# Kernel tuning notes

Hardware: AMD Instinct MI355X
Metric: run time of the kernel (lower is better)

Reference implementation:

```python
import jax, jax.numpy as jnp
import numpy as np

B, A, L, M, E = 4096, 64, 16, 4, 10
K = (4, 16, 32)
Q = (2, 4, 6)
P = (32, 128, 256)


def setup_inputs() -> dict:
    key = jax.random.key(0)
    ks = iter(jax.random.split(key, 32))
    inp = {}
    inp['x'] = jax.random.normal(next(ks), (B, A, L, M), dtype=jnp.float32)
    inp['y'] = jax.random.uniform(next(ks), (B, E), dtype=jnp.float32)
    inp['w1'] = jax.random.normal(next(ks), (E, K[0], Q[0], A), dtype=jnp.float32) / (K[0] * Q[0])
    inp['w2'] = jax.random.normal(next(ks), (E, K[1], Q[1], A), dtype=jnp.float32) / (K[1] * Q[1])
    inp['w3'] = jax.random.normal(next(ks), (E, K[2], Q[2], A), dtype=jnp.float32) / (K[2] * Q[2])
    inp['coeff1'] = jax.random.normal(next(ks), (P[0],), dtype=jnp.float32)
    inp['coeff2'] = jax.random.normal(next(ks), (P[1],), dtype=jnp.float32)
    inp['coeff3'] = jax.random.normal(next(ks), (P[2],), dtype=jnp.float32)
    ri = lambda n, hi: jax.random.randint(next(ks), (n,), 0, hi, dtype=jnp.int32)
    inp['i1'] = ri(P[0], L); inp['l1'] = ri(P[0], M)
    inp['k1'] = ri(P[0], K[0]); inp['q1'] = ri(P[0], Q[0])
    inp['i2'] = ri(P[1], L); inp['j2'] = ri(P[1], L)
    inp['l2'] = ri(P[1], M); inp['m2'] = ri(P[1], M)
    inp['k2'] = ri(P[1], K[1]); inp['q2'] = ri(P[1], Q[1])
    inp['i3'] = ri(P[2], L); inp['j3'] = ri(P[2], L); inp['f3'] = ri(P[2], L)
    inp['l3'] = ri(P[2], M); inp['m3'] = ri(P[2], M); inp['g3'] = ri(P[2], M)
    inp['k3'] = ri(P[2], K[2]); inp['q3'] = ri(P[2], Q[2])
    return inp


def _forward(x, y, w1, w2, w3, coeff1, coeff2, coeff3,
             i1, l1, k1, q1,
             i2, j2, l2, m2, k2, q2,
             i3, j3, f3, l3, m3, g3, k3, q3):
    # element-mixed weights: [B, K, Q, A]
    wy1 = jnp.einsum('ekqa,be->bkqa', w1, y)
    wy2 = jnp.einsum('ekqa,be->bkqa', w2, y)
    wy3 = jnp.einsum('ekqa,be->bkqa', w3, y)
    # sparse path contraction (equivalent to dense 'ik,lq,ekqa,bail,be->ba' etc.)
    g1 = jnp.transpose(wy1[:, k1, q1, :], (0, 2, 1))          # [B, A, P1]
    t1 = jnp.einsum('bap,p->ba', x[:, :, i1, l1] * g1, coeff1)
    g2 = jnp.transpose(wy2[:, k2, q2, :], (0, 2, 1))          # [B, A, P2]
    t2 = jnp.einsum('bap,p->ba', x[:, :, i2, l2] * x[:, :, j2, m2] * g2, coeff2)
    g3_ = jnp.transpose(wy3[:, k3, q3, :], (0, 2, 1))         # [B, A, P3]
    t3 = jnp.einsum('bap,p->ba',
                    x[:, :, i3, l3] * x[:, :, j3, m3] * x[:, :, f3, g3] * g3_,
                    coeff3)
    return t1 + t2 + t3  # [B, A] (scalar irrep_out -> flattened view)


def reference(x, y, w1, w2, w3, coeff1, coeff2, coeff3,
              i1, l1, k1, q1,
              i2, j2, l2, m2, k2, q2,
              i3, j3, f3, l3, m3, g3, k3, q3):
    return _forward(x, y, w1, w2, w3, coeff1, coeff2, coeff3,
                    i1, l1, k1, q1,
                    i2, j2, l2, m2, k2, q2,
                    i3, j3, f3, l3, m3, g3, k3, q3)
```

## Files before the change

### kernel.cpp

```cpp
#include <hip/hip_runtime.h>
#include <hip/hip_bf16.h>

typedef _Float16 f16x8 __attribute__((ext_vector_type(8)));
typedef _Float16 f16x4 __attribute__((ext_vector_type(4)));
typedef float    f32x4 __attribute__((ext_vector_type(4)));

constexpr int BB  = 4096;
constexpr int AA  = 64;
constexpr int ED  = 10;
constexpr int P1N = 32, P2N = 128, P3N = 256;
constexpr int PT  = 416;
constexpr int NKS = 13;
constexpr int BCH = 64;
constexpr int NCH = 4;

__global__ void build_tables_kernel(
    const float* __restrict__ w1, const float* __restrict__ w2, const float* __restrict__ w3,
    const float* __restrict__ c1, const float* __restrict__ c2, const float* __restrict__ c3,
    const int* __restrict__ k1, const int* __restrict__ q1,
    const int* __restrict__ k2, const int* __restrict__ q2,
    const int* __restrict__ k3, const int* __restrict__ q3,
    const int* __restrict__ i1, const int* __restrict__ l1,
    const int* __restrict__ i2, const int* __restrict__ j2,
    const int* __restrict__ l2, const int* __restrict__ m2,
    const int* __restrict__ i3, const int* __restrict__ j3,
    const int* __restrict__ f3, const int* __restrict__ l3,
    const int* __restrict__ m3, const int* __restrict__ g3,
    _Float16* __restrict__ cwb, unsigned* __restrict__ idxs) {
  if (blockIdx.x == AA * NKS) {
    for (int p = threadIdx.x; p < PT; p += 64) {
      unsigned sa, sb = 64, sc = 64;
      if (p < P1N) {
        sa = i1[p] * 4 + l1[p];
      } else if (p < P1N + P2N) {
        int pp = p - P1N;
        sa = i2[pp] * 4 + l2[pp];
        sb = j2[pp] * 4 + m2[pp];
      } else {
        int pp = p - P1N - P2N;
        sa = i3[pp] * 4 + l3[pp];
        sb = j3[pp] * 4 + m3[pp];
        sc = f3[pp] * 4 + g3[pp];
      }
      idxs[p] = (sa * 8) | ((sb * 8) << 10) | ((sc * 8) << 20);
    }
    return;
  }
  const int a  = blockIdx.x & 63;
  const int ks = blockIdx.x >> 6;
  const int l  = threadIdx.x;
  const int grp = l >> 4, e = l & 15;
  const int aq = a >> 2, ch = a & 3;
  _Float16* dst = cwb + ((((size_t)aq * NKS + ks) * 64 + l) * 4 + ch) * 8;
  #pragma unroll
  for (int j = 0; j < 8; ++j) {
    const int p = ks * 32 + grp * 8 + j;
    float v = 0.f;
    if (e < ED) {
      const float* w; float coeff; int k, q, K, Q;
      if (p < P1N)            { w = w1; coeff = c1[p]; k = k1[p]; q = q1[p]; K = 4;  Q = 2; }
      else if (p < P1N + P2N) { int pp = p - P1N;       w = w2; coeff = c2[pp]; k = k2[pp]; q = q2[pp]; K = 16; Q = 4; }
      else                    { int pp = p - P1N - P2N; w = w3; coeff = c3[pp]; k = k3[pp]; q = q3[pp]; K = 32; Q = 6; }
      v = coeff * w[(((size_t)e * K + k) * Q + q) * AA + a];
    }
    dst[j] = (_Float16)v;
  }
}

template <int NF, int KS>
__device__ __forceinline__ void kstep(
    const char* __restrict__ rowb, const uint4* ip,
    const f16x8* __restrict__ cwq,
    f32x4& ac0, f32x4& ac1, f32x4& ac2, f32x4& ac3) {
  const uint4 iA = ip[KS * 8 + 0];
  const uint4 iB = ip[KS * 8 + 1];
  const f16x8* c = cwq + KS * 256;
  const f16x8 b0 = c[0];
  const f16x8 b1 = c[1];
  const f16x8 b2 = c[2];
  const f16x8 b3 = c[3];
  const unsigned pks[8] = {iA.x, iA.y, iA.z, iA.w, iB.x, iB.y, iB.z, iB.w};
  f16x8 af0, af1, af2, af3;
  #pragma unroll
  for (int jh = 0; jh < 2; ++jh) {
    f16x4 g0[4], g1[4], g2[4];
    #pragma unroll
    for (int j = 0; j < 4; ++j) {
      const unsigned pk = pks[jh * 4 + j];
      g0[j] = *(const f16x4*)(rowb + (pk & 1023u));
      if (NF >= 2) g1[j] = *(const f16x4*)(rowb + ((pk >> 10) & 1023u));
      if (NF >= 3) g2[j] = *(const f16x4*)(rowb + (pk >> 20));
    }
    #pragma unroll
    for (int j = 0; j < 4; ++j) {
      f16x4 v = g0[j];
      if (NF >= 2) v = v * g1[j];
      if (NF >= 3) v = v * g2[j];
      const int jj = jh * 4 + j;
      af0[jj] = v[0]; af1[jj] = v[1]; af2[jj] = v[2]; af3[jj] = v[3];
    }
  }
  ac0 = __builtin_amdgcn_mfma_f32_16x16x32_f16(af0, b0, ac0, 0, 0, 0);
  ac1 = __builtin_amdgcn_mfma_f32_16x16x32_f16(af1, b1, ac1, 0, 0, 0);
  ac2 = __builtin_amdgcn_mfma_f32_16x16x32_f16(af2, b2, ac2, 0, 0, 0);
  ac3 = __builtin_amdgcn_mfma_f32_16x16x32_f16(af3, b3, ac3, 0, 0, 0);
}

__global__ __launch_bounds__(256, 4)
void contract_kernel(const float* __restrict__ x, const float* __restrict__ y,
                     const unsigned* __restrict__ idxs,
                     const f16x8* __restrict__ cwb,
                     float* __restrict__ out) {
  __shared__ f16x4 xls[BCH][65];
  __shared__ float yls[BCH][17];
  __shared__ uint4 ils[PT / 4];

  const int t  = threadIdx.x;
  const int aq = blockIdx.x & 15;
  const int a0 = aq * NCH;
  const int b0 = (blockIdx.x >> 4) * BCH;
  const int wv = t >> 6, l = t & 63, grp = l >> 4, er = l & 15;
  const int r0 = wv * 16;

  {
    const uint4* gip = (const uint4*)idxs;
    for (int u = l; u < PT / 4; u += 64) ils[u] = gip[u];
  }

  #pragma unroll
  for (int i = 0; i < 4; ++i) {
    const int row = r0 + i * 4 + (l >> 4);
    const int s   = (l & 15) * 4;
    const float* xb = x + (size_t)(b0 + row) * 4096 + a0 * 64 + s;
    const float4 L0 = *(const float4*)(xb);
    const float4 L1 = *(const float4*)(xb + 64);
    const float4 L2 = *(const float4*)(xb + 128);
    const float4 L3 = *(const float4*)(xb + 192);
    f16x4 v0, v1, v2, v3;
    v0[0] = (_Float16)L0.x; v0[1] = (_Float16)L1.x; v0[2] = (_Float16)L2.x; v0[3] = (_Float16)L3.x;
    v1[0] = (_Float16)L0.y; v1[1] = (_Float16)L1.y; v1[2] = (_Float16)L2.y; v1[3] = (_Float16)L3.y;
    v2[0] = (_Float16)L0.z; v2[1] = (_Float16)L1.z; v2[2] = (_Float16)L2.z; v2[3] = (_Float16)L3.z;
    v3[0] = (_Float16)L0.w; v3[1] = (_Float16)L1.w; v3[2] = (_Float16)L2.w; v3[3] = (_Float16)L3.w;
    xls[row][s + 0] = v0;
    xls[row][s + 1] = v1;
    xls[row][s + 2] = v2;
    xls[row][s + 3] = v3;
  }
  if (l < 16) {
    f16x4 one;
    one[0] = one[1] = one[2] = one[3] = (_Float16)1.0f;
    xls[r0 + l][64] = one;
    const float* yb = y + (size_t)(b0 + r0 + l) * ED;
    #pragma unroll
    for (int e = 0; e < ED; ++e) yls[r0 + l][e] = yb[e];
    #pragma unroll
    for (int e = ED; e < 16; ++e) yls[r0 + l][e] = 0.f;
  }

  const char* __restrict__ rowb = (const char*)&xls[r0 + er][0];
  const f16x8* __restrict__ cwq = cwb + (size_t)aq * NKS * 256 + (size_t)l * 4;
  const uint4* ip = &ils[grp * 2];

  f32x4 a0A = {0.f, 0.f, 0.f, 0.f}, a1A = a0A, a2A = a0A, a3A = a0A;
  f32x4 a0B = a0A, a1B = a0A, a2B = a0A, a3B = a0A;

  #define SA(NF, KS) kstep<NF, KS>(rowb, ip, cwq, a0A, a1A, a2A, a3A)
  #define SB(NF, KS) kstep<NF, KS>(rowb, ip, cwq, a0B, a1B, a2B, a3B)
  SA(1, 0);  SB(3, 7);
  SA(2, 1);  SB(3, 8);
  SA(2, 2);  SB(3, 9);
  SA(2, 3);  SB(3, 10);
  SA(2, 4);  SB(3, 11);
  SA(3, 5);  SB(3, 12);
  SA(3, 6);
  #undef SA
  #undef SB

  const f32x4 ac0 = a0A + a0B;
  const f32x4 ac1 = a1A + a1B;
  const f32x4 ac2 = a2A + a2B;
  const f32x4 ac3 = a3A + a3B;

  #pragma unroll
  for (int c = 0; c < NCH; ++c) {
    const f32x4 acc = c == 0 ? ac0 : c == 1 ? ac1 : c == 2 ? ac2 : ac3;
    float s0 = acc[0] * yls[r0 + grp * 4 + 0][er];
    float s1 = acc[1] * yls[r0 + grp * 4 + 1][er];
    float s2 = acc[2] * yls[r0 + grp * 4 + 2][er];
    float s3 = acc[3] * yls[r0 + grp * 4 + 3][er];
    #pragma unroll
    for (int m = 1; m < 16; m <<= 1) {
      s0 += __shfl_xor(s0, m);
      s1 += __shfl_xor(s1, m);
      s2 += __shfl_xor(s2, m);
      s3 += __shfl_xor(s3, m);
    }
    if (er < 4) {
      const float sv = er == 0 ? s0 : er == 1 ? s1 : er == 2 ? s2 : s3;
      out[(size_t)(b0 + r0 + grp * 4 + er) * AA + (a0 + c)] = sv;
    }
  }
}

extern "C" void kernel_launch(void* const* d_in, const int* in_sizes, int n_in,
                              void* d_out, int out_size, void* d_ws, size_t ws_size,
                              hipStream_t stream) {
  const float* x  = (const float*)d_in[0];
  const float* y  = (const float*)d_in[1];
  const float* w1 = (const float*)d_in[2];
  const float* w2 = (const float*)d_in[3];
  const float* w3 = (const float*)d_in[4];
  const float* c1 = (const float*)d_in[5];
  const float* c2 = (const float*)d_in[6];
  const float* c3 = (const float*)d_in[7];
  const int* i1 = (const int*)d_in[8];
  const int* l1 = (const int*)d_in[9];
  const int* k1 = (const int*)d_in[10];
  const int* q1 = (const int*)d_in[11];
  const int* i2 = (const int*)d_in[12];
  const int* j2 = (const int*)d_in[13];
  const int* l2 = (const int*)d_in[14];
  const int* m2 = (const int*)d_in[15];
  const int* k2 = (const int*)d_in[16];
  const int* q2 = (const int*)d_in[17];
  const int* i3 = (const int*)d_in[18];
  const int* j3 = (const int*)d_in[19];
  const int* f3 = (const int*)d_in[20];
  const int* l3 = (const int*)d_in[21];
  const int* m3 = (const int*)d_in[22];
  const int* g3 = (const int*)d_in[23];
  const int* k3 = (const int*)d_in[24];
  const int* q3 = (const int*)d_in[25];

  unsigned*  idxs = (unsigned*)d_ws;
  _Float16*  cwb  = (_Float16*)((char*)d_ws + 4096);

  build_tables_kernel<<<AA * NKS + 1, 64, 0, stream>>>(
      w1, w2, w3, c1, c2, c3, k1, q1, k2, q2, k3, q3,
      i1, l1, i2, j2, l2, m2, i3, j3, f3, l3, m3, g3, cwb, idxs);
  contract_kernel<<<(AA / NCH) * (BB / BCH), 256, 0, stream>>>(
      x, y, idxs, (const f16x8*)cwb, (float*)d_out);
}
```

Before: 36.43 us.

## Widen channel tile to eight per block with f16x8 gathers

Each block now handles 8 output channels instead of 4. x is packed in LDS as f16x8 per slot, so each index gather and multiply feeds eight MFMA chains instead of four, spreading index decode and LDS gather work over more channels. The weight table layout and packed index encoding are widened to match, and the y LDS staging and ones slot are removed, with y now read directly from global. The two interleaved accumulator sets become one. The trade-off is half as many blocks, larger dynamic LDS (set via a function attribute on every launch), and launch bounds lowered to 2 blocks, which cuts occupancy and latency hiding.

Measured after the change: 46.99 us. +29.0%, slower.

```diff
diff --git a/kernel.cpp b/kernel.cpp
--- a/kernel.cpp
+++ b/kernel.cpp
@@ -2,7 +2,6 @@
 #include <hip/hip_bf16.h>
 
 typedef _Float16 f16x8 __attribute__((ext_vector_type(8)));
-typedef _Float16 f16x4 __attribute__((ext_vector_type(4)));
 typedef float    f32x4 __attribute__((ext_vector_type(4)));
 
 constexpr int BB  = 4096;
@@ -12,7 +11,11 @@
 constexpr int PT  = 416;
 constexpr int NKS = 13;
 constexpr int BCH = 64;
-constexpr int NCH = 4;
+constexpr int NCH = 8;
+
+constexpr int    ROWSLOTS  = 65;
+constexpr size_t XLS_BYTES = (size_t)BCH * ROWSLOTS * 16;
+constexpr size_t LDS_BYTES = XLS_BYTES + PT * 4;
 
 __global__ void build_tables_kernel(
     const float* __restrict__ w1, const float* __restrict__ w2, const float* __restrict__ w3,
@@ -29,7 +32,7 @@
     _Float16* __restrict__ cwb, unsigned* __restrict__ idxs) {
   if (blockIdx.x == AA * NKS) {
     for (int p = threadIdx.x; p < PT; p += 64) {
-      unsigned sa, sb = 64, sc = 64;
+      unsigned sa, sb = 0, sc = 0;
       if (p < P1N) {
         sa = i1[p] * 4 + l1[p];
       } else if (p < P1N + P2N) {
@@ -42,7 +45,7 @@
         sb = j3[pp] * 4 + m3[pp];
         sc = f3[pp] * 4 + g3[pp];
       }
-      idxs[p] = (sa * 8) | ((sb * 8) << 10) | ((sc * 8) << 20);
+      idxs[p] = (sa * 16) | ((sb * 16) << 11) | (sc << 22);
     }
     return;
   }
@@ -50,8 +53,8 @@
   const int ks = blockIdx.x >> 6;
   const int l  = threadIdx.x;
   const int grp = l >> 4, e = l & 15;
-  const int aq = a >> 2, ch = a & 3;
-  _Float16* dst = cwb + ((((size_t)aq * NKS + ks) * 64 + l) * 4 + ch) * 8;
+  const int aq = a >> 3, ch = a & 7;
+  _Float16* dst = cwb + ((((size_t)aq * NKS + ks) * 64 + l) * 8 + ch) * 8;
   #pragma unroll
   for (int j = 0; j < 8; ++j) {
     const int p = ks * 32 + grp * 8 + j;
@@ -69,56 +72,54 @@
 
 template <int NF, int KS>
 __device__ __forceinline__ void kstep(
-    const char* __restrict__ rowb, const uint4* ip,
-    const f16x8* __restrict__ cwq,
-    f32x4& ac0, f32x4& ac1, f32x4& ac2, f32x4& ac3) {
+    const char* rowb, const uint4* ip,
+    const f16x8* __restrict__ cwq, f32x4 (&ac)[NCH]) {
   const uint4 iA = ip[KS * 8 + 0];
   const uint4 iB = ip[KS * 8 + 1];
-  const f16x8* c = cwq + KS * 256;
-  const f16x8 b0 = c[0];
-  const f16x8 b1 = c[1];
-  const f16x8 b2 = c[2];
-  const f16x8 b3 = c[3];
+  const f16x8* c = cwq + KS * 512;
+  f16x8 bfr[NCH];
+  #pragma unroll
+  for (int ch = 0; ch < NCH; ++ch) bfr[ch] = c[ch];
   const unsigned pks[8] = {iA.x, iA.y, iA.z, iA.w, iB.x, iB.y, iB.z, iB.w};
-  f16x8 af0, af1, af2, af3;
+  f16x8 af[NCH];
   #pragma unroll
   for (int jh = 0; jh < 2; ++jh) {
-    f16x4 g0[4], g1[4], g2[4];
+    f16x8 g0[4], g1[4], g2[4];
     #pragma unroll
     for (int j = 0; j < 4; ++j) {
       const unsigned pk = pks[jh * 4 + j];
-      g0[j] = *(const f16x4*)(rowb + (pk & 1023u));
-      if (NF >= 2) g1[j] = *(const f16x4*)(rowb + ((pk >> 10) & 1023u));
-      if (NF >= 3) g2[j] = *(const f16x4*)(rowb + (pk >> 20));
+      g0[j] = *(const f16x8*)(rowb + (pk & 2047u));
+      if (NF >= 2) g1[j] = *(const f16x8*)(rowb + ((pk >> 11) & 2047u));
+      if (NF >= 3) g2[j] = *(const f16x8*)(rowb + ((pk >> 22) << 4));
     }
     #pragma unroll
     for (int j = 0; j < 4; ++j) {
-      f16x4 v = g0[j];
+      f16x8 v = g0[j];
       if (NF >= 2) v = v * g1[j];
       if (NF >= 3) v = v * g2[j];
       const int jj = jh * 4 + j;
-      af0[jj] = v[0]; af1[jj] = v[1]; af2[jj] = v[2]; af3[jj] = v[3];
-    }
-  }
-  ac0 = __builtin_amdgcn_mfma_f32_16x16x32_f16(af0, b0, ac0, 0, 0, 0);
-  ac1 = __builtin_amdgcn_mfma_f32_16x16x32_f16(af1, b1, ac1, 0, 0, 0);
-  ac2 = __builtin_amdgcn_mfma_f32_16x16x32_f16(af2, b2, ac2, 0, 0, 0);
-  ac3 = __builtin_amdgcn_mfma_f32_16x16x32_f16(af3, b3, ac3, 0, 0, 0);
-}
-
-__global__ __launch_bounds__(256, 4)
+      #pragma unroll
+      for (int ch = 0; ch < NCH; ++ch) af[ch][jj] = v[ch];
+    }
+  }
+  #pragma unroll
+  for (int ch = 0; ch < NCH; ++ch)
+    ac[ch] = __builtin_amdgcn_mfma_f32_16x16x32_f16(af[ch], bfr[ch], ac[ch], 0, 0, 0);
+}
+
+__global__ __launch_bounds__(256, 2)
 void contract_kernel(const float* __restrict__ x, const float* __restrict__ y,
                      const unsigned* __restrict__ idxs,
                      const f16x8* __restrict__ cwb,
                      float* __restrict__ out) {
-  __shared__ f16x4 xls[BCH][65];
-  __shared__ float yls[BCH][17];
-  __shared__ uint4 ils[PT / 4];
+  extern __shared__ char lds[];
+  f16x8 (*xls)[ROWSLOTS] = (f16x8(*)[ROWSLOTS])lds;
+  uint4* ils = (uint4*)(lds + XLS_BYTES);
 
   const int t  = threadIdx.x;
-  const int aq = blockIdx.x & 15;
+  const int aq = blockIdx.x & 7;
   const int a0 = aq * NCH;
-  const int b0 = (blockIdx.x >> 4) * BCH;
+  const int b0 = (blockIdx.x >> 3) * BCH;
   const int wv = t >> 6, l = t & 63, grp = l >> 4, er = l & 15;
   const int r0 = wv * 16;
 
@@ -132,62 +133,45 @@
     const int row = r0 + i * 4 + (l >> 4);
     const int s   = (l & 15) * 4;
     const float* xb = x + (size_t)(b0 + row) * 4096 + a0 * 64 + s;
-    const float4 L0 = *(const float4*)(xb);
-    const float4 L1 = *(const float4*)(xb + 64);
-    const float4 L2 = *(const float4*)(xb + 128);
-    const float4 L3 = *(const float4*)(xb + 192);
-    f16x4 v0, v1, v2, v3;
-    v0[0] = (_Float16)L0.x; v0[1] = (_Float16)L1.x; v0[2] = (_Float16)L2.x; v0[3] = (_Float16)L3.x;
-    v1[0] = (_Float16)L0.y; v1[1] = (_Float16)L1.y; v1[2] = (_Float16)L2.y; v1[3] = (_Float16)L3.y;
-    v2[0] = (_Float16)L0.z; v2[1] = (_Float16)L1.z; v2[2] = (_Float16)L2.z; v2[3] = (_Float16)L3.z;
-    v3[0] = (_Float16)L0.w; v3[1] = (_Float16)L1.w; v3[2] = (_Float16)L2.w; v3[3] = (_Float16)L3.w;
-    xls[row][s + 0] = v0;
-    xls[row][s + 1] = v1;
-    xls[row][s + 2] = v2;
-    xls[row][s + 3] = v3;
-  }
-  if (l < 16) {
-    f16x4 one;
-    one[0] = one[1] = one[2] = one[3] = (_Float16)1.0f;
-    xls[r0 + l][64] = one;
-    const float* yb = y + (size_t)(b0 + r0 + l) * ED;
-    #pragma unroll
-    for (int e = 0; e < ED; ++e) yls[r0 + l][e] = yb[e];
-    #pragma unroll
-    for (int e = ED; e < 16; ++e) yls[r0 + l][e] = 0.f;
-  }
-
-  const char* __restrict__ rowb = (const char*)&xls[r0 + er][0];
-  const f16x8* __restrict__ cwq = cwb + (size_t)aq * NKS * 256 + (size_t)l * 4;
+    float4 L[NCH];
+    #pragma unroll
+    for (int ch = 0; ch < NCH; ++ch) L[ch] = *(const float4*)(xb + 64 * ch);
+    #pragma unroll
+    for (int k = 0; k < 4; ++k) {
+      f16x8 v;
+      #pragma unroll
+      for (int ch = 0; ch < NCH; ++ch) v[ch] = (_Float16)((&L[ch].x)[k]);
+      xls[row][s + k] = v;
+    }
+  }
+
+  const char* rowb = (const char*)&xls[r0 + er][0];
+  const f16x8* __restrict__ cwq = cwb + (size_t)aq * NKS * 512 + (size_t)l * 8;
   const uint4* ip = &ils[grp * 2];
 
-  f32x4 a0A = {0.f, 0.f, 0.f, 0.f}, a1A = a0A, a2A = a0A, a3A = a0A;
-  f32x4 a0B = a0A, a1B = a0A, a2B = a0A, a3B = a0A;
-
-  #define SA(NF, KS) kstep<NF, KS>(rowb, ip, cwq, a0A, a1A, a2A, a3A)
-  #define SB(NF, KS) kstep<NF, KS>(rowb, ip, cwq, a0B, a1B, a2B, a3B)
-  SA(1, 0);  SB(3, 7);
-  SA(2, 1);  SB(3, 8);
-  SA(2, 2);  SB(3, 9);
-  SA(2, 3);  SB(3, 10);
-  SA(2, 4);  SB(3, 11);
-  SA(3, 5);  SB(3, 12);
-  SA(3, 6);
-  #undef SA
-  #undef SB
-
-  const f32x4 ac0 = a0A + a0B;
-  const f32x4 ac1 = a1A + a1B;
-  const f32x4 ac2 = a2A + a2B;
-  const f32x4 ac3 = a3A + a3B;
+  f32x4 ac[NCH];
+  #pragma unroll
+  for (int ch = 0; ch < NCH; ++ch) ac[ch] = f32x4{0.f, 0.f, 0.f, 0.f};
+
+  #define STEP(NF, KS) kstep<NF, KS>(rowb, ip, cwq, ac)
+  STEP(1, 0);
+  STEP(2, 1); STEP(2, 2); STEP(2, 3); STEP(2, 4);
+  STEP(3, 5); STEP(3, 6); STEP(3, 7); STEP(3, 8);
+  STEP(3, 9); STEP(3, 10); STEP(3, 11); STEP(3, 12);
+  #undef STEP
+
+  const int rbase = b0 + r0 + grp * 4;
+  float ye[4];
+  #pragma unroll
+  for (int r = 0; r < 4; ++r)
+    ye[r] = (er < ED) ? y[(size_t)(rbase + r) * ED + er] : 0.f;
 
   #pragma unroll
   for (int c = 0; c < NCH; ++c) {
-    const f32x4 acc = c == 0 ? ac0 : c == 1 ? ac1 : c == 2 ? ac2 : ac3;
-    float s0 = acc[0] * yls[r0 + grp * 4 + 0][er];
-    float s1 = acc[1] * yls[r0 + grp * 4 + 1][er];
-    float s2 = acc[2] * yls[r0 + grp * 4 + 2][er];
-    float s3 = acc[3] * yls[r0 + grp * 4 + 3][er];
+    float s0 = ac[c][0] * ye[0];
+    float s1 = ac[c][1] * ye[1];
+    float s2 = ac[c][2] * ye[2];
+    float s3 = ac[c][3] * ye[3];
     #pragma unroll
     for (int m = 1; m < 16; m <<= 1) {
       s0 += __shfl_xor(s0, m);
@@ -197,7 +181,7 @@
     }
     if (er < 4) {
       const float sv = er == 0 ? s0 : er == 1 ? s1 : er == 2 ? s2 : s3;
-      out[(size_t)(b0 + r0 + grp * 4 + er) * AA + (a0 + c)] = sv;
+      out[(size_t)(rbase + er) * AA + (a0 + c)] = sv;
     }
   }
 }
@@ -238,6 +222,10 @@
   build_tables_kernel<<<AA * NKS + 1, 64, 0, stream>>>(
       w1, w2, w3, c1, c2, c3, k1, q1, k2, q2, k3, q3,
       i1, l1, i2, j2, l2, m2, i3, j3, f3, l3, m3, g3, cwb, idxs);
-  contract_kernel<<<(AA / NCH) * (BB / BCH), 256, 0, stream>>>(
+
+  hipFuncSetAttribute((const void*)contract_kernel,
+                      hipFuncAttributeMaxDynamicSharedMemorySize,
+                      (int)LDS_BYTES);
+  contract_kernel<<<(AA / NCH) * (BB / BCH), 256, LDS_BYTES, stream>>>(
       x, y, idxs, (const f16x8*)cwb, (float*)d_out);
 }
```
